# Optimization experiments

Hardware: AMD Instinct MI355X
Metric: run time of the kernel (lower is better)

The kernel has to match this reference:

```python
import jax, jax.numpy as jnp
import numpy as np

SEQ_LEN, BATCH, TAG = 512, 1024, 64
START_IDX, END_IDX = 0, 1
NEG_INF = -10000.0


def setup_inputs() -> dict:
    key = jax.random.key(0)
    k1, k2, k3 = jax.random.split(key, 3)
    feats = jax.random.normal(k1, (SEQ_LEN, BATCH, TAG), dtype=jnp.float32)
    # variable-length sequences: valid prefix lengths in [SEQ_LEN//2, SEQ_LEN]
    lens = jax.random.randint(k2, (BATCH,), SEQ_LEN // 2, SEQ_LEN + 1)
    mask = (jnp.arange(SEQ_LEN)[:, None] < lens[None, :]).astype(jnp.float32)  # (S, B)
    # transition ~ xavier_normal_ then clamp START row / END column (reset_parameters)
    std = float(np.sqrt(2.0 / (TAG + TAG)))
    transition = jax.random.normal(k3, (TAG, TAG), dtype=jnp.float32) * std
    transition = transition.at[START_IDX, :].set(NEG_INF)
    transition = transition.at[:, END_IDX].set(NEG_INF)
    return {"feats": feats, "mask": mask, "transition": transition}


def reference(feats, mask, transition):
    # feats: (S, B, T), mask: (S, B), transition: (T, T) [next_tag, prev_tag]
    S, B, T = feats.shape
    alpha0 = jnp.full((B, T), NEG_INF, dtype=feats.dtype).at[:, START_IDX].set(0.0)

    def step(alpha, xs):
        feat, m = xs  # feat: (B, T), m: (B,)
        # alpha_score[b, next, prev] = alpha[b, prev] + transition[next, prev] + feat[b, next]
        score = alpha[:, None, :] + transition[None, :, :] + feat[:, :, None]
        new_alpha = jax.nn.logsumexp(score, axis=-1)  # (B, T)
        m = m[:, None]
        alpha = new_alpha * m + alpha * (1.0 - m)
        return alpha, None

    alpha, _ = jax.lax.scan(step, alpha0, (feats, mask))
    alpha = alpha + transition[END_IDX][None, :]
    return jax.nn.logsumexp(alpha, axis=-1)  # (B,)
```

## Files before the change

kernel.cpp:

```cpp
#include <hip/hip_runtime.h>

namespace {
constexpr int S_LEN = 512;
constexpr int BATCH = 1024;
constexpr int TAG = 64;
constexpr int START_IDX = 0;
constexpr int END_IDX = 1;
constexpr float NEG_INF = -10000.0f;
constexpr int CHUNK = 64;
constexpr float LN2F = 0.69314718055994530942f;

typedef float v2f __attribute__((ext_vector_type(2)));
typedef float v4f __attribute__((ext_vector_type(4)));

typedef const __attribute__((address_space(1))) void* gas_ptr;
typedef __attribute__((address_space(3))) void* las_ptr;

__device__ inline void gld_lds16(const float* g, float* l) {
  __builtin_amdgcn_global_load_lds((gas_ptr)(const void*)g, (las_ptr)(void*)l, 16, 0, 0);
}
}

__global__ __launch_bounds__(64, 1) void crf_fwd_kernel(
    const float* __restrict__ feats,
    const float* __restrict__ mask,
    const float* __restrict__ trans,
    float* __restrict__ out) {
  const int b = blockIdx.x;
  const int lane = threadIdx.x;

  __shared__ __align__(16) float fchunk[2][CHUNK * TAG];
  __shared__ __align__(16) float p_lds[TAG];

  int L;
  {
    float sum = 0.0f;
#pragma unroll
    for (int k = 0; k < S_LEN / 64; ++k) sum += mask[(size_t)(lane + 64 * k) * BATCH + b];
#pragma unroll
    for (int off = 32; off >= 1; off >>= 1) sum += __shfl_xor(sum, off, 64);
    L = (int)(sum + 0.5f);
  }

  v2f E[TAG / 2];
  {
    const float* row = trans + lane * TAG;
#pragma unroll
    for (int k = 0; k < TAG / 4; ++k) {
      v4f tv;
      __builtin_memcpy(&tv, row + 4 * k, sizeof(v4f));
      E[2 * k]     = v2f{__expf(tv.x), __expf(tv.y)};
      E[2 * k + 1] = v2f{__expf(tv.z), __expf(tv.w)};
    }
  }

  const float* gstage0 =
      feats + ((size_t)(lane >> 4) * BATCH + b) * TAG + ((lane & 15) << 2);

  auto stage_chunk = [&](int base_s, int nb) {
    const float* g0 = gstage0 + (size_t)base_s * (BATCH * TAG);
#pragma unroll
    for (int q = 0; q < 16; ++q) {
      gld_lds16(g0 + (size_t)(4 * q) * (BATCH * TAG), &fchunk[nb][q * 256]);
    }
  };

  float p = (lane == START_IDX) ? 1.0f : 0.0f;
  int etot = 0;

  p_lds[lane] = p;
  __builtin_amdgcn_wave_barrier();

  stage_chunk(0, 0);
  asm volatile("s_waitcnt vmcnt(0)" ::: "memory");
  __builtin_amdgcn_sched_barrier(0);
  __builtin_amdgcn_wave_barrier();

  for (int c = 0;; ++c) {
    const int base = c * CHUNK;
    int n = L - base;
    if (n <= 0) break;
    if (n > CHUNK) n = CHUNK;

    const int nbase = base + CHUNK;
    if (nbase < S_LEN) stage_chunk(nbase, (c + 1) & 1);

    const float* fb = &fchunk[c & 1][0];

    auto step = [&](int i) {
      const float fcur = fb[i * TAG + lane];

      const unsigned pb = __builtin_amdgcn_readlane(__float_as_uint(p), 2);
      const unsigned eb = (pb == 0u) ? 127u : (pb >> 23);
      etot += (int)eb - 127;
      const float scale = __uint_as_float((254u - eb) << 23);
      const float cg = __expf(fcur) * scale;

      v2f acc0 = {0.f, 0.f}, acc1 = {0.f, 0.f}, acc2 = {0.f, 0.f}, acc3 = {0.f, 0.f};
      v2f acc4 = {0.f, 0.f}, acc5 = {0.f, 0.f}, acc6 = {0.f, 0.f}, acc7 = {0.f, 0.f};
#pragma unroll
      for (int k = 0; k < 4; ++k) {
        v4f q0, q1, q2, q3;
        __builtin_memcpy(&q0, p_lds + 16 * k + 0,  sizeof(v4f));
        __builtin_memcpy(&q1, p_lds + 16 * k + 4,  sizeof(v4f));
        __builtin_memcpy(&q2, p_lds + 16 * k + 8,  sizeof(v4f));
        __builtin_memcpy(&q3, p_lds + 16 * k + 12, sizeof(v4f));
        acc0 += v2f{q0.x, q0.y} * E[8 * k + 0];
        acc1 += v2f{q0.z, q0.w} * E[8 * k + 1];
        acc2 += v2f{q1.x, q1.y} * E[8 * k + 2];
        acc3 += v2f{q1.z, q1.w} * E[8 * k + 3];
        acc4 += v2f{q2.x, q2.y} * E[8 * k + 4];
        acc5 += v2f{q2.z, q2.w} * E[8 * k + 5];
        acc6 += v2f{q3.x, q3.y} * E[8 * k + 6];
        acc7 += v2f{q3.z, q3.w} * E[8 * k + 7];
      }
      const v2f s0 = (acc0 + acc1) + (acc2 + acc3);
      const v2f s1 = (acc4 + acc5) + (acc6 + acc7);
      const v2f st = s0 + s1;
      const float t = st.x + st.y;

      p = t * cg;

      __builtin_amdgcn_wave_barrier();
      p_lds[lane] = p;
      __builtin_amdgcn_wave_barrier();
    };

    if (n == CHUNK) {
#pragma unroll 8
      for (int i = 0; i < CHUNK; ++i) step(i);
    } else {
      for (int i = 0; i < n; ++i) step(i);
      break;
    }

    if (nbase >= L) break;

    asm volatile("s_waitcnt vmcnt(0)" ::: "memory");
    __builtin_amdgcn_sched_barrier(0);
    __builtin_amdgcn_wave_barrier();
  }

  asm volatile("s_waitcnt vmcnt(0)" ::: "memory");

  {
    const float a = (float)etot * LN2F + __logf(p) + trans[END_IDX * TAG + lane];
    float mx = a;
#pragma unroll
    for (int off = 32; off >= 1; off >>= 1) mx = fmaxf(mx, __shfl_xor(mx, off, 64));
    float e = __expf(a - mx);
#pragma unroll
    for (int off = 32; off >= 1; off >>= 1) e += __shfl_xor(e, off, 64);
    if (lane == 0) out[b] = mx + __logf(e);
  }
}

extern "C" void kernel_launch(void* const* d_in, const int* in_sizes, int n_in,
                              void* d_out, int out_size, void* d_ws, size_t ws_size,
                              hipStream_t stream) {
  const float* feats = (const float*)d_in[0];
  const float* mask = (const float*)d_in[1];
  const float* trans = (const float*)d_in[2];
  float* out = (float*)d_out;
  crf_fwd_kernel<<<dim3(BATCH), dim3(64), 0, stream>>>(feats, mask, trans, out);
}
```

Before: 258.0 us.

## Broadcast recurrence state via readlane instead of LDS round trip

Each time step used to write the 64-element scaled probability vector to LDS, barrier, and read it back with vector loads for a packed dot product. The new code feeds the operands with 64 v_readlane broadcasts of p from lanes into scalar FMAs, which removes the LDS store/load latency and wave barriers from the serial dependency chain. It also batches eight feature loads and exps per group so they come off the per-step critical path. The trade is many more issued instructions per step (64 readlanes plus 64 scalar FMAs instead of 16 b128 LDS loads plus 32 packed FMAs), and possible SGPR-to-VALU hazard stalls.

```diff
diff --git a/kernel.cpp b/kernel.cpp
--- a/kernel.cpp
+++ b/kernel.cpp
@@ -30,7 +30,6 @@
   const int lane = threadIdx.x;
 
   __shared__ __align__(16) float fchunk[2][CHUNK * TAG];
-  __shared__ __align__(16) float p_lds[TAG];
 
   int L;
   {
@@ -42,15 +41,17 @@
     L = (int)(sum + 0.5f);
   }
 
-  v2f E[TAG / 2];
+  float Ee[TAG];
   {
     const float* row = trans + lane * TAG;
 #pragma unroll
     for (int k = 0; k < TAG / 4; ++k) {
       v4f tv;
       __builtin_memcpy(&tv, row + 4 * k, sizeof(v4f));
-      E[2 * k]     = v2f{__expf(tv.x), __expf(tv.y)};
-      E[2 * k + 1] = v2f{__expf(tv.z), __expf(tv.w)};
+      Ee[4 * k + 0] = __expf(tv.x);
+      Ee[4 * k + 1] = __expf(tv.y);
+      Ee[4 * k + 2] = __expf(tv.z);
+      Ee[4 * k + 3] = __expf(tv.w);
     }
   }
 
@@ -68,13 +69,36 @@
   float p = (lane == START_IDX) ? 1.0f : 0.0f;
   int etot = 0;
 
-  p_lds[lane] = p;
-  __builtin_amdgcn_wave_barrier();
-
   stage_chunk(0, 0);
   asm volatile("s_waitcnt vmcnt(0)" ::: "memory");
   __builtin_amdgcn_sched_barrier(0);
   __builtin_amdgcn_wave_barrier();
+
+  auto step = [&](float ex) {
+    const unsigned pu = __float_as_uint(p);
+
+    const unsigned pb = __builtin_amdgcn_readlane(pu, 2);
+    const unsigned eb = (pb == 0u) ? 127u : (pb >> 23);
+    etot += (int)eb - 127;
+    const float scale = __uint_as_float((254u - eb) << 23);
+    const float cg = ex * scale;
+
+    float a0 = 0.f, a1 = 0.f, a2 = 0.f, a3 = 0.f;
+    float a4 = 0.f, a5 = 0.f, a6 = 0.f, a7 = 0.f;
+#pragma unroll
+    for (int k = 0; k < TAG; k += 8) {
+      a0 = __builtin_fmaf(__uint_as_float(__builtin_amdgcn_readlane(pu, k + 0)), Ee[k + 0], a0);
+      a1 = __builtin_fmaf(__uint_as_float(__builtin_amdgcn_readlane(pu, k + 1)), Ee[k + 1], a1);
+      a2 = __builtin_fmaf(__uint_as_float(__builtin_amdgcn_readlane(pu, k + 2)), Ee[k + 2], a2);
+      a3 = __builtin_fmaf(__uint_as_float(__builtin_amdgcn_readlane(pu, k + 3)), Ee[k + 3], a3);
+      a4 = __builtin_fmaf(__uint_as_float(__builtin_amdgcn_readlane(pu, k + 4)), Ee[k + 4], a4);
+      a5 = __builtin_fmaf(__uint_as_float(__builtin_amdgcn_readlane(pu, k + 5)), Ee[k + 5], a5);
+      a6 = __builtin_fmaf(__uint_as_float(__builtin_amdgcn_readlane(pu, k + 6)), Ee[k + 6], a6);
+      a7 = __builtin_fmaf(__uint_as_float(__builtin_amdgcn_readlane(pu, k + 7)), Ee[k + 7], a7);
+    }
+    const float t = ((a0 + a1) + (a2 + a3)) + ((a4 + a5) + (a6 + a7));
+    p = t * cg;
+  };
 
   for (int c = 0;; ++c) {
     const int base = c * CHUNK;
@@ -87,50 +111,24 @@
 
     const float* fb = &fchunk[c & 1][0];
 
-    auto step = [&](int i) {
-      const float fcur = fb[i * TAG + lane];
-
-      const unsigned pb = __builtin_amdgcn_readlane(__float_as_uint(p), 2);
-      const unsigned eb = (pb == 0u) ? 127u : (pb >> 23);
-      etot += (int)eb - 127;
-      const float scale = __uint_as_float((254u - eb) << 23);
-      const float cg = __expf(fcur) * scale;
-
-      v2f acc0 = {0.f, 0.f}, acc1 = {0.f, 0.f}, acc2 = {0.f, 0.f}, acc3 = {0.f, 0.f};
-      v2f acc4 = {0.f, 0.f}, acc5 = {0.f, 0.f}, acc6 = {0.f, 0.f}, acc7 = {0.f, 0.f};
+    auto group8 = [&](int s0) {
+      float ex[8];
 #pragma unroll
-      for (int k = 0; k < 4; ++k) {
-        v4f q0, q1, q2, q3;
-        __builtin_memcpy(&q0, p_lds + 16 * k + 0,  sizeof(v4f));
-        __builtin_memcpy(&q1, p_lds + 16 * k + 4,  sizeof(v4f));
-        __builtin_memcpy(&q2, p_lds + 16 * k + 8,  sizeof(v4f));
-        __builtin_memcpy(&q3, p_lds + 16 * k + 12, sizeof(v4f));
-        acc0 += v2f{q0.x, q0.y} * E[8 * k + 0];
-        acc1 += v2f{q0.z, q0.w} * E[8 * k + 1];
-        acc2 += v2f{q1.x, q1.y} * E[8 * k + 2];
-        acc3 += v2f{q1.z, q1.w} * E[8 * k + 3];
-        acc4 += v2f{q2.x, q2.y} * E[8 * k + 4];
-        acc5 += v2f{q2.z, q2.w} * E[8 * k + 5];
-        acc6 += v2f{q3.x, q3.y} * E[8 * k + 6];
-        acc7 += v2f{q3.z, q3.w} * E[8 * k + 7];
-      }
-      const v2f s0 = (acc0 + acc1) + (acc2 + acc3);
-      const v2f s1 = (acc4 + acc5) + (acc6 + acc7);
-      const v2f st = s0 + s1;
-      const float t = st.x + st.y;
-
-      p = t * cg;
-
-      __builtin_amdgcn_wave_barrier();
-      p_lds[lane] = p;
-      __builtin_amdgcn_wave_barrier();
+      for (int i = 0; i < 8; ++i) ex[i] = fb[(s0 + i) * TAG + lane];
+#pragma unroll
+      for (int i = 0; i < 8; ++i) ex[i] = __expf(ex[i]);
+#pragma unroll
+      for (int i = 0; i < 8; ++i) step(ex[i]);
     };
 
     if (n == CHUNK) {
-#pragma unroll 8
-      for (int i = 0; i < CHUNK; ++i) step(i);
+      for (int g = 0; g < CHUNK / 8; ++g) group8(8 * g);
     } else {
-      for (int i = 0; i < n; ++i) step(i);
+      const int full = n >> 3;
+      for (int g = 0; g < full; ++g) group8(8 * g);
+      for (int i = full * 8; i < n; ++i) {
+        step(__expf(fb[i * TAG + lane]));
+      }
       break;
     }
 
```

New measurement: 271.6 us. 5.3% more time.
